# Kernel tuning notes

Hardware: AMD Instinct MI355X
Metric: run time of the kernel (lower is better)

## Reference

```python
import jax, jax.numpy as jnp
import numpy as np

B, S, H = 16, 8192, 256

def setup_inputs() -> dict:
    key = jax.random.key(0)
    k1, k2, k3, k4, k5 = jax.random.split(key, 5)
    hidden = jax.random.normal(k1, (B, 1, H), dtype=jnp.float32)
    encoder_outputs = jax.random.normal(k2, (B, S, 2 * H), dtype=jnp.float32)
    attn_w = jax.random.normal(k3, (H, 3 * H), dtype=jnp.float32) / np.sqrt(3 * H)
    attn_b = jax.random.normal(k4, (H,), dtype=jnp.float32) * 0.01
    v = jax.random.uniform(k5, (H,), dtype=jnp.float32)
    return {"hidden": hidden, "encoder_outputs": encoder_outputs,
            "attn_w": attn_w, "attn_b": attn_b, "v": v}

def reference(hidden, encoder_outputs, attn_w, attn_b, v):
    # Vectorized form of the per-timestep loop:
    # energies[b, s] = sum_h v[h] * tanh(Linear(cat(hidden[b], enc[b, s])))
    b, s, _ = encoder_outputs.shape
    h_bcast = jnp.broadcast_to(hidden, (b, s, hidden.shape[-1]))  # [B,S,H]
    combined = jnp.concatenate([h_bcast, encoder_outputs], axis=-1)  # [B,S,3H]
    energy = jnp.tanh(jnp.einsum('bsk,hk->bsh', combined, attn_w) + attn_b)  # [B,S,H]
    attn_energies = jnp.einsum('bsh,h->bs', energy, v)  # [B,S]
    return jax.nn.softmax(attn_energies, axis=1)[:, None, :]  # [B,1,S]
```

## Files before the change

### kernel.cpp

```cpp
#include <hip/hip_runtime.h>
#include <hip/hip_bf16.h>

#define B_ 16
#define S_ 8192
#define H_ 256
#define K_ 512
#define NT_ 16

typedef __attribute__((ext_vector_type(8))) short bf16x8;
typedef __attribute__((ext_vector_type(4))) float f32x4;

static __device__ __forceinline__ unsigned short f2bf(float x) {
    __hip_bfloat16 h = __float2bfloat16(x);
    unsigned short r;
    __builtin_memcpy(&r, &h, 2);
    return r;
}

static __device__ __forceinline__ bf16x8 pack8(float4 f0, float4 f1) {
    bf16x8 r;
    r[0] = (short)f2bf(f0.x); r[1] = (short)f2bf(f0.y);
    r[2] = (short)f2bf(f0.z); r[3] = (short)f2bf(f0.w);
    r[4] = (short)f2bf(f1.x); r[5] = (short)f2bf(f1.y);
    r[6] = (short)f2bf(f1.z); r[7] = (short)f2bf(f1.w);
    return r;
}

static __device__ __forceinline__ float fast_tanh(float x) {
    x = fminf(15.f, fmaxf(-15.f, x));
    float e = __expf(2.f * x);
    return 1.f - 2.f * __builtin_amdgcn_rcpf(e + 1.f);
}

__global__ __launch_bounds__(1024) void prep_kernel(const float* __restrict__ w,
                                                    const float* __restrict__ bias,
                                                    const float* __restrict__ hid,
                                                    bf16x8* __restrict__ wfrag,
                                                    float* __restrict__ q) {
    int blk = blockIdx.x;
    int tid = threadIdx.x;
    if (blk < 16) {
        int slot = blk * 1024 + tid;
        int lane = slot & 63;
        int nt   = (slot >> 6) & 15;
        int ks   = slot >> 10;
        int n  = (nt << 4) + (lane & 15);
        int k0 = (ks << 5) + ((lane >> 4) << 3);
        const float* src = w + n * 768 + 256 + k0;
        float4 f0 = *(const float4*)(src);
        float4 f1 = *(const float4*)(src + 4);
        wfrag[slot] = pack8(f0, f1);
    } else {
        int b = blk - 16;
        int h = tid >> 2, part = tid & 3;
        const float* wr = w + h * 768 + part * 64;
        const float* hb = hid + b * H_ + part * 64;
        float acc = 0.f;
#pragma unroll
        for (int i = 0; i < 16; ++i) {
            float4 a = *(const float4*)(wr + i * 4);
            float4 x = *(const float4*)(hb + i * 4);
            acc += a.x * x.x + a.y * x.y + a.z * x.z + a.w * x.w;
        }
        acc += __shfl_xor(acc, 1);
        acc += __shfl_xor(acc, 2);
        if (part == 0) q[b * H_ + h] = acc + bias[h];
    }
}

__global__ __launch_bounds__(256) void energy_kernel(const float* __restrict__ enc,
                                                     const bf16x8* __restrict__ wfrag,
                                                     const float* __restrict__ qv,
                                                     const float* __restrict__ vv,
                                                     float* __restrict__ ener) {
    const int bid  = blockIdx.x;
    const int b    = bid >> 7;
    const int s0   = (bid & 127) * 64;
    const int tid  = threadIdx.x;
    const int lane = tid & 63;
    const int wv   = tid >> 6;
    const int lr   = lane & 15;
    const int lg   = lane >> 4;
    const int r0   = s0 + wv * 16;

    const float* arow = enc + ((size_t)(b * S_ + r0 + lr)) * K_ + lg * 8;
    const bf16x8* wbase = wfrag + lane;

    f32x4 acc[NT_];
#pragma unroll
    for (int nt = 0; nt < NT_; ++nt) acc[nt] = (f32x4){0.f, 0.f, 0.f, 0.f};

#pragma unroll 2
    for (int ks = 0; ks < 16; ++ks) {
        float4 f0 = *(const float4*)(arow + ks * 32);
        float4 f1 = *(const float4*)(arow + ks * 32 + 4);
        bf16x8 a = pack8(f0, f1);
#pragma unroll
        for (int nt = 0; nt < NT_; ++nt) {
            bf16x8 bf = wbase[(ks * 16 + nt) * 64];
            acc[nt] = __builtin_amdgcn_mfma_f32_16x16x32_bf16(a, bf, acc[nt], 0, 0, 0);
        }
    }

    const float* qb = qv + b * H_;
    float e[4] = {0.f, 0.f, 0.f, 0.f};
#pragma unroll
    for (int nt = 0; nt < NT_; ++nt) {
        float qn = qb[nt * 16 + lr];
        float vn = vv[nt * 16 + lr];
#pragma unroll
        for (int j = 0; j < 4; ++j)
            e[j] += vn * fast_tanh(qn + acc[nt][j]);
    }
#pragma unroll
    for (int j = 0; j < 4; ++j) {
        e[j] += __shfl_xor(e[j], 1);
        e[j] += __shfl_xor(e[j], 2);
        e[j] += __shfl_xor(e[j], 4);
        e[j] += __shfl_xor(e[j], 8);
    }
    if (lr == 0) {
        float* op = ener + b * S_ + r0 + lg * 4;
        op[0] = e[0]; op[1] = e[1]; op[2] = e[2]; op[3] = e[3];
    }
}

__global__ __launch_bounds__(1024) void softmax_kernel(const float* __restrict__ ener,
                                                       float* __restrict__ out) {
    __shared__ float redm[16], reds[16];
    int b = blockIdx.x, tid = threadIdx.x;
    int lane = tid & 63, wv = tid >> 6;
    const float* e = ener + b * S_;
    float v[8];
#pragma unroll
    for (int i = 0; i < 8; ++i) v[i] = e[i * 1024 + tid];
    float m = v[0];
#pragma unroll
    for (int i = 1; i < 8; ++i) m = fmaxf(m, v[i]);
#pragma unroll
    for (int msk = 1; msk < 64; msk <<= 1) m = fmaxf(m, __shfl_xor(m, msk));
    if (lane == 0) redm[wv] = m;
    __syncthreads();
    float M = redm[0];
#pragma unroll
    for (int i = 1; i < 16; ++i) M = fmaxf(M, redm[i]);
    float s = 0.f;
#pragma unroll
    for (int i = 0; i < 8; ++i) { v[i] = __expf(v[i] - M); s += v[i]; }
#pragma unroll
    for (int msk = 1; msk < 64; msk <<= 1) s += __shfl_xor(s, msk);
    if (lane == 0) reds[wv] = s;
    __syncthreads();
    float T = 0.f;
#pragma unroll
    for (int i = 0; i < 16; ++i) T += reds[i];
    float inv = 1.0f / T;
    float* ob = out + b * S_;
#pragma unroll
    for (int i = 0; i < 8; ++i) ob[i * 1024 + tid] = v[i] * inv;
}

extern "C" void kernel_launch(void* const* d_in, const int* in_sizes, int n_in,
                              void* d_out, int out_size, void* d_ws, size_t ws_size,
                              hipStream_t stream) {
    const float* hidden = (const float*)d_in[0];
    const float* enc    = (const float*)d_in[1];
    const float* attn_w = (const float*)d_in[2];
    const float* attn_b = (const float*)d_in[3];
    const float* v      = (const float*)d_in[4];
    float* out = (float*)d_out;

    char* ws = (char*)d_ws;
    bf16x8* wfrag = (bf16x8*)ws;
    float*  q     = (float*)(ws + 262144);
    float*  ener  = (float*)(ws + 262144 + 16384);

    prep_kernel<<<32, 1024, 0, stream>>>(attn_w, attn_b, hidden, wfrag, q);
    energy_kernel<<<B_ * (S_ / 64), 256, 0, stream>>>(enc, wfrag, q, v, ener);
    softmax_kernel<<<B_, 1024, 0, stream>>>(ener, out);
}
```

Baseline: 454.4 us.

## Switch energy GEMM to 32x32 MFMA with LDS double-buffered weights

Reworks the energy kernel to use 32x32x16 bf16 MFMA tiles with 128 rows per block. The weight fragments are streamed into a 64KB double-buffered LDS via direct global-to-LDS loads instead of being read from global memory by every wave. The activation rows are prefetched four k-steps ahead in registers. This cuts repeated global weight traffic and raises math per load, but the larger LDS footprint and the 16-wide accumulators per tile raise register and LDS pressure, which may lower occupancy.

```diff
diff --git a/kernel.cpp b/kernel.cpp
--- a/kernel.cpp
+++ b/kernel.cpp
@@ -5,10 +5,12 @@
 #define S_ 8192
 #define H_ 256
 #define K_ 512
-#define NT_ 16
-
-typedef __attribute__((ext_vector_type(8))) short bf16x8;
-typedef __attribute__((ext_vector_type(4))) float f32x4;
+#define NT32_ 8
+#define NKS_ 32
+
+typedef __attribute__((ext_vector_type(8)))  short bf16x8;
+typedef __attribute__((ext_vector_type(16))) float f32x16;
+typedef unsigned int u32;
 
 static __device__ __forceinline__ unsigned short f2bf(float x) {
     __hip_bfloat16 h = __float2bfloat16(x);
@@ -30,6 +32,11 @@
     x = fminf(15.f, fmaxf(-15.f, x));
     float e = __expf(2.f * x);
     return 1.f - 2.f * __builtin_amdgcn_rcpf(e + 1.f);
+}
+
+static __device__ __forceinline__ void gload_lds16(const void* g, void* l) {
+    __builtin_amdgcn_global_load_lds((const __attribute__((address_space(1))) u32*)g,
+                                     (__attribute__((address_space(3))) u32*)l, 16, 0, 0);
 }
 
 __global__ __launch_bounds__(1024) void prep_kernel(const float* __restrict__ w,
@@ -42,10 +49,10 @@
     if (blk < 16) {
         int slot = blk * 1024 + tid;
         int lane = slot & 63;
-        int nt   = (slot >> 6) & 15;
-        int ks   = slot >> 10;
-        int n  = (nt << 4) + (lane & 15);
-        int k0 = (ks << 5) + ((lane >> 4) << 3);
+        int nt   = (slot >> 6) & 7;
+        int ks   = slot >> 9;
+        int n  = (nt << 5) + (lane & 31);
+        int k0 = (ks << 4) + ((lane >> 5) << 3);
         const float* src = w + n * 768 + 256 + k0;
         float4 f0 = *(const float4*)(src);
         float4 f1 = *(const float4*)(src + 4);
@@ -69,59 +76,99 @@
 }
 
 __global__ __launch_bounds__(256) void energy_kernel(const float* __restrict__ enc,
-                                                     const bf16x8* __restrict__ wfrag,
+                                                     const char* __restrict__ wfrag,
                                                      const float* __restrict__ qv,
                                                      const float* __restrict__ vv,
                                                      float* __restrict__ ener) {
+    __shared__ char Bs[2][32768];
+
     const int bid  = blockIdx.x;
-    const int b    = bid >> 7;
-    const int s0   = (bid & 127) * 64;
+    const int b    = bid >> 6;
+    const int s0   = (bid & 63) * 128;
     const int tid  = threadIdx.x;
     const int lane = tid & 63;
     const int wv   = tid >> 6;
-    const int lr   = lane & 15;
-    const int lg   = lane >> 4;
-    const int r0   = s0 + wv * 16;
-
-    const float* arow = enc + ((size_t)(b * S_ + r0 + lr)) * K_ + lg * 8;
-    const bf16x8* wbase = wfrag + lane;
-
-    f32x4 acc[NT_];
-#pragma unroll
-    for (int nt = 0; nt < NT_; ++nt) acc[nt] = (f32x4){0.f, 0.f, 0.f, 0.f};
-
-#pragma unroll 2
-    for (int ks = 0; ks < 16; ++ks) {
-        float4 f0 = *(const float4*)(arow + ks * 32);
-        float4 f1 = *(const float4*)(arow + ks * 32 + 4);
-        bf16x8 a = pack8(f0, f1);
-#pragma unroll
-        for (int nt = 0; nt < NT_; ++nt) {
-            bf16x8 bf = wbase[(ks * 16 + nt) * 64];
-            acc[nt] = __builtin_amdgcn_mfma_f32_16x16x32_bf16(a, bf, acc[nt], 0, 0, 0);
+    const int lc   = lane & 31;
+    const int hi   = lane >> 5;
+    const int r0   = s0 + wv * 32;
+
+    const float* arow = enc + ((size_t)(b * S_ + r0 + lc)) * K_ + hi * 8;
+
+#pragma unroll
+    for (int i = 0; i < 8; ++i) {
+        int off = i * 4096 + tid * 16;
+        gload_lds16(wfrag + off,         Bs[0] + off);
+        gload_lds16(wfrag + 32768 + off, Bs[1] + off);
+    }
+
+    float4 fbuf[4][2];
+#pragma unroll
+    for (int p = 0; p < 4; ++p) {
+        fbuf[p][0] = *(const float4*)(arow + p * 16);
+        fbuf[p][1] = *(const float4*)(arow + p * 16 + 4);
+    }
+
+    f32x16 acc[NT32_];
+#pragma unroll
+    for (int nt = 0; nt < NT32_; ++nt)
+#pragma unroll
+        for (int r = 0; r < 16; ++r) acc[nt][r] = 0.f;
+
+    __syncthreads();
+
+#pragma unroll
+    for (int c = 0; c < 8; ++c) {
+        const char* Bb = Bs[c & 1];
+#pragma unroll
+        for (int ksl = 0; ksl < 4; ++ksl) {
+            const int ks = c * 4 + ksl;
+            bf16x8 a = pack8(fbuf[ks & 3][0], fbuf[ks & 3][1]);
+            if (ks + 4 < NKS_) {
+                fbuf[ks & 3][0] = *(const float4*)(arow + (ks + 4) * 16);
+                fbuf[ks & 3][1] = *(const float4*)(arow + (ks + 4) * 16 + 4);
+            }
+#pragma unroll
+            for (int nt = 0; nt < NT32_; ++nt) {
+                bf16x8 bfr = *(const bf16x8*)(Bb + ksl * 8192 + nt * 1024 + lane * 16);
+                acc[nt] = __builtin_amdgcn_mfma_f32_32x32x16_bf16(a, bfr, acc[nt], 0, 0, 0);
+            }
         }
+        __syncthreads();
+        if (c < 6) {
+            const char* src = wfrag + (c + 2) * 32768;
+#pragma unroll
+            for (int i = 0; i < 8; ++i) {
+                int off = i * 4096 + tid * 16;
+                gload_lds16(src + off, Bs[c & 1] + off);
+            }
+        }
     }
 
     const float* qb = qv + b * H_;
-    float e[4] = {0.f, 0.f, 0.f, 0.f};
-#pragma unroll
-    for (int nt = 0; nt < NT_; ++nt) {
-        float qn = qb[nt * 16 + lr];
-        float vn = vv[nt * 16 + lr];
-#pragma unroll
-        for (int j = 0; j < 4; ++j)
-            e[j] += vn * fast_tanh(qn + acc[nt][j]);
-    }
-#pragma unroll
-    for (int j = 0; j < 4; ++j) {
-        e[j] += __shfl_xor(e[j], 1);
-        e[j] += __shfl_xor(e[j], 2);
-        e[j] += __shfl_xor(e[j], 4);
-        e[j] += __shfl_xor(e[j], 8);
-    }
-    if (lr == 0) {
-        float* op = ener + b * S_ + r0 + lg * 4;
-        op[0] = e[0]; op[1] = e[1]; op[2] = e[2]; op[3] = e[3];
+    float er[16];
+#pragma unroll
+    for (int r = 0; r < 16; ++r) er[r] = 0.f;
+#pragma unroll
+    for (int nt = 0; nt < NT32_; ++nt) {
+        float qn = qb[nt * 32 + lc];
+        float vn = vv[nt * 32 + lc];
+#pragma unroll
+        for (int r = 0; r < 16; ++r)
+            er[r] += vn * fast_tanh(qn + acc[nt][r]);
+    }
+#pragma unroll
+    for (int r = 0; r < 16; ++r) {
+        er[r] += __shfl_xor(er[r], 1);
+        er[r] += __shfl_xor(er[r], 2);
+        er[r] += __shfl_xor(er[r], 4);
+        er[r] += __shfl_xor(er[r], 8);
+        er[r] += __shfl_xor(er[r], 16);
+    }
+    if (lc == 0) {
+        float* op = ener + b * S_ + r0;
+#pragma unroll
+        for (int r = 0; r < 16; ++r)
+            op[(r & 3) + 8 * (r >> 2) + 4 * hi] = er[r];
     }
 }
 
@@ -176,6 +223,6 @@
     float*  ener  = (float*)(ws + 262144 + 16384);
 
     prep_kernel<<<32, 1024, 0, stream>>>(attn_w, attn_b, hidden, wfrag, q);
-    energy_kernel<<<B_ * (S_ / 64), 256, 0, stream>>>(enc, wfrag, q, v, ener);
+    energy_kernel<<<B_ * (S_ / 128), 256, 0, stream>>>(enc, (const char*)wfrag, q, v, ener);
     softmax_kernel<<<B_, 1024, 0, stream>>>(ener, out);
 }
```

Measured after the change: 409.5 us. 1.11x faster.
